# Optimization experiments

Hardware: AMD Instinct MI355X
Metric: run time of the kernel (lower is better)

Reference implementation:

```python
import jax, jax.numpy as jnp
import numpy as np

HEADS = 16
GRID_SIZE = 5      # efficient-KAN default
SPLINE_ORDER = 3   # efficient-KAN default


def _grid(in_features, dtype):
    # grid_range = [-1, 1]
    h = 2.0 / GRID_SIZE
    g = jnp.arange(-SPLINE_ORDER, GRID_SIZE + SPLINE_ORDER + 1, dtype=dtype) * h - 1.0
    return jnp.broadcast_to(g, (in_features, g.shape[0]))  # (in, G)


def _b_splines(x, grid):
    # x: (N, in), grid: (in, G); Cox-de Boor recursion
    xg = x[:, :, None]
    bases = ((xg >= grid[:, :-1]) & (xg < grid[:, 1:])).astype(x.dtype)
    for k in range(1, SPLINE_ORDER + 1):
        bases = ((xg - grid[:, :-(k + 1)]) / (grid[:, k:-1] - grid[:, :-(k + 1)]) * bases[:, :, :-1]
                 + (grid[:, k + 1:] - xg) / (grid[:, k + 1:] - grid[:, 1:-k]) * bases[:, :, 1:])
    return bases  # (N, in, GRID_SIZE + SPLINE_ORDER)


def _kan_linear(x, base_w, spline_w, spline_scaler):
    grid = _grid(x.shape[-1], x.dtype)
    base = jax.nn.silu(x) @ base_w.T                      # (N, out)
    b = _b_splines(x, grid)                               # (N, in, K)
    sw = spline_w * spline_scaler[..., None]              # (out, in, K)
    return base + jnp.einsum('nik,oik->no', b, sw)


def setup_inputs():
    key = jax.random.key(0)
    S, H = 2048, 1024
    hd = H // HEADS
    K = GRID_SIZE + SPLINE_ORDER
    ks = jax.random.split(key, 6)
    x = jax.random.normal(ks[0], (S, H), jnp.float32)
    base_w = jax.random.normal(ks[1], (3 * H, H), jnp.float32) / np.float32(np.sqrt(H))
    spline_w = jax.random.normal(ks[2], (3 * H, H, K), jnp.float32) * 0.1
    spline_scaler = 1.0 + 0.1 * jax.random.normal(ks[3], (3 * H, H), jnp.float32)
    out_w = jax.random.normal(ks[4], (H, H), jnp.float32) / np.float32(np.sqrt(H))
    out_b = jnp.zeros((H,), jnp.float32)
    # RoPE rotation matrix (unit complex), theta = 10000
    t = jnp.arange(S, dtype=jnp.float32)
    freqs = 1.0 / (10000.0 ** (jnp.arange(0, hd, 2, dtype=jnp.float32) / hd))
    ang = jnp.outer(t, freqs)  # (S, hd//2)
    return {"x": x, "base_w": base_w, "spline_w": spline_w,
            "spline_scaler": spline_scaler, "out_w": out_w, "out_b": out_b,
            "rot_cos": jnp.cos(ang), "rot_sin": jnp.sin(ang)}


def reference(x, base_w, spline_w, spline_scaler, out_w, out_b, rot_cos, rot_sin):
    S, H = x.shape
    hd = H // HEADS
    qkv = _kan_linear(x, base_w, spline_w, spline_scaler)          # (S, 3H)
    qkv = qkv.reshape(1, S, HEADS, 3 * hd).transpose(0, 2, 1, 3)   # (1,h,S,3d)
    q, k, v = jnp.split(qkv, 3, axis=-1)                           # each (1,h,S,d)

    def rope(t):
        tp = t.reshape(1, HEADS, S, hd // 2, 2)
        c = rot_cos[None, None]
        s = rot_sin[None, None]
        re = tp[..., 0] * c - tp[..., 1] * s
        im = tp[..., 0] * s + tp[..., 1] * c
        return jnp.stack([re, im], axis=-1).reshape(1, HEADS, S, hd)

    q, k = rope(q), rope(k)
    scores = jnp.einsum('bhqd,bhkd->bhqk', q, k) / np.float32(np.sqrt(hd))
    attn = jax.nn.softmax(scores, axis=-1)
    ctx = jnp.einsum('bhqk,bhkd->bhqd', attn, v)
    ctx = ctx.transpose(0, 2, 1, 3).reshape(1, S, H)
    return ctx @ out_w.T + out_b
```

## Files before the change

kernel.cpp:

```cpp
#include <hip/hip_runtime.h>

typedef unsigned short u16;
typedef __bf16 bf16x8 __attribute__((ext_vector_type(8)));
typedef float f32x4 __attribute__((ext_vector_type(4)));

#define S_LEN 2048
#define NHEADS 16
#define HD 64
#define HDIM 1024
#define QKVN 3072
#define KAUG 9216

__device__ __forceinline__ u16 f2bf(float f) {
  union { float f; unsigned u; } v; v.f = f;
  unsigned r = v.u + 0x7fffu + ((v.u >> 16) & 1u);
  return (u16)(r >> 16);
}

typedef __attribute__((address_space(1))) const unsigned int gas_u32;
typedef __attribute__((address_space(3))) unsigned int las_u32;
__device__ __forceinline__ void gload_lds16(const void* g, void* l) {
  __builtin_amdgcn_global_load_lds((gas_u32*)g, (las_u32*)l, 16, 0, 0);
}

__global__ void prep_a_kernel(const float* __restrict__ x, u16* __restrict__ Aaug) {
  int idx = blockIdx.x * 256 + threadIdx.x;
  int n = idx >> 10, i = idx & 1023;
  float xv = x[idx];
  float sil = xv / (1.0f + __expf(-xv));
  Aaug[(size_t)n * KAUG + i] = f2bf(sil);

  float b[11];
#pragma unroll
  for (int j = 0; j < 11; ++j) {
    float t0 = 0.4f * (float)(j - 3) - 1.0f;
    float t1 = 0.4f * (float)(j - 2) - 1.0f;
    b[j] = (xv >= t0 && xv < t1) ? 1.0f : 0.0f;
  }
#pragma unroll
  for (int k = 1; k <= 3; ++k) {
#pragma unroll
    for (int j = 0; j < 10; ++j) {
      if (j + k < 11) {
        float tj   = 0.4f * (float)(j - 3) - 1.0f;
        float tjk  = tj + 0.4f * (float)k;
        float tj1  = tj + 0.4f;
        float tjk1 = tjk + 0.4f;
        b[j] = (xv - tj) / (tjk - tj) * b[j] + (tjk1 - xv) / (tjk1 - tj1) * b[j + 1];
      }
    }
  }
  u16 t[8];
#pragma unroll
  for (int j = 0; j < 8; ++j) t[j] = f2bf(b[j]);
  uint4 pk;
  pk.x = (unsigned)t[0] | ((unsigned)t[1] << 16);
  pk.y = (unsigned)t[2] | ((unsigned)t[3] << 16);
  pk.z = (unsigned)t[4] | ((unsigned)t[5] << 16);
  pk.w = (unsigned)t[6] | ((unsigned)t[7] << 16);
  *reinterpret_cast<uint4*>(&Aaug[(size_t)n * KAUG + 1024 + i * 8]) = pk;
}

__global__ void prep_w_kernel(const float* __restrict__ bw, const float* __restrict__ sw,
                              const float* __restrict__ sc, u16* __restrict__ Waug) {
  int idx = blockIdx.x * 256 + threadIdx.x;
  int o = idx >> 10, i = idx & 1023;
  Waug[(size_t)o * KAUG + i] = f2bf(bw[idx]);
  float s = sc[idx];
  const float4* sp = reinterpret_cast<const float4*>(sw + (size_t)idx * 8);
  float4 a = sp[0], b = sp[1];
  uint4 pk;
  pk.x = (unsigned)f2bf(a.x * s) | ((unsigned)f2bf(a.y * s) << 16);
  pk.y = (unsigned)f2bf(a.z * s) | ((unsigned)f2bf(a.w * s) << 16);
  pk.z = (unsigned)f2bf(b.x * s) | ((unsigned)f2bf(b.y * s) << 16);
  pk.w = (unsigned)f2bf(b.z * s) | ((unsigned)f2bf(b.w * s) << 16);
  *reinterpret_cast<uint4*>(&Waug[(size_t)o * KAUG + 1024 + i * 8]) = pk;
}

__global__ void prep_ow_kernel(const float* __restrict__ ow, u16* __restrict__ owbf) {
  int idx = blockIdx.x * 256 + threadIdx.x;
  float4 v = reinterpret_cast<const float4*>(ow)[idx];
  uint2 pk;
  pk.x = (unsigned)f2bf(v.x) | ((unsigned)f2bf(v.y) << 16);
  pk.y = (unsigned)f2bf(v.z) | ((unsigned)f2bf(v.w) << 16);
  reinterpret_cast<uint2*>(owbf)[idx] = pk;
}

__global__ __launch_bounds__(256) void gemm_bt(
    const u16* __restrict__ A, const u16* __restrict__ B, float* __restrict__ C,
    int M, int N, int K, int Ksp, const float* __restrict__ bias)
{
  __shared__ u16 As[128 * 32];
  __shared__ u16 Bs[128 * 32];
  const int tid = threadIdx.x;
  const int lane = tid & 63;
  const int w = tid >> 6;
  const int wr = w >> 1, wc = w & 1;
  const int bm = blockIdx.y, bn = blockIdx.x;
  const int row0 = bm * 128, col0 = bn * 128;
  const int lr = lane & 15, lg = lane >> 4;
  const int kbeg = blockIdx.z * Ksp;
  const int kend = kbeg + Ksp;
  float* Cz = C + (size_t)blockIdx.z * M * N;

  f32x4 acc[4][4];
#pragma unroll
  for (int m = 0; m < 4; ++m)
#pragma unroll
    for (int n = 0; n < 4; ++n) acc[m][n] = (f32x4){0.f, 0.f, 0.f, 0.f};

  const int arow = tid >> 2;
  const int kch  = tid & 3;

  for (int k0 = kbeg; k0 < kend; k0 += 32) {
    const u16* ga0 = A + (size_t)(row0 + arow) * K + k0 + kch * 8;
    const u16* ga1 = ga0 + (size_t)64 * K;
    gload_lds16(ga0, &As[tid * 8]);
    gload_lds16(ga1, &As[2048 + tid * 8]);
    const u16* gb0 = B + (size_t)(col0 + arow) * K + k0 + kch * 8;
    const u16* gb1 = gb0 + (size_t)64 * K;
    gload_lds16(gb0, &Bs[tid * 8]);
    gload_lds16(gb1, &Bs[2048 + tid * 8]);
    __syncthreads();

    bf16x8 af[4], bf[4];
#pragma unroll
    for (int m = 0; m < 4; ++m) {
      int r = wr * 64 + m * 16 + lr;
      af[m] = *reinterpret_cast<const bf16x8*>(&As[r * 32 + lg * 8]);
    }
#pragma unroll
    for (int n = 0; n < 4; ++n) {
      int r = wc * 64 + n * 16 + lr;
      bf[n] = *reinterpret_cast<const bf16x8*>(&Bs[r * 32 + lg * 8]);
    }
#pragma unroll
    for (int m = 0; m < 4; ++m)
#pragma unroll
      for (int n = 0; n < 4; ++n)
        acc[m][n] = __builtin_amdgcn_mfma_f32_16x16x32_bf16(af[m], bf[n], acc[m][n], 0, 0, 0);
    __syncthreads();
  }

#pragma unroll
  for (int m = 0; m < 4; ++m) {
    int row = row0 + wr * 64 + m * 16 + lg * 4;
#pragma unroll
    for (int n = 0; n < 4; ++n) {
      int col = col0 + wc * 64 + n * 16 + lr;
      float bv = bias ? bias[col] : 0.f;
#pragma unroll
      for (int j = 0; j < 4; ++j)
        Cz[(size_t)(row + j) * N + col] = acc[m][n][j] + bv;
    }
  }
}

__global__ void rope_kernel(const float* __restrict__ qkv0, const float* __restrict__ qkv1,
                            const float* __restrict__ rc, const float* __restrict__ rs,
                            u16* __restrict__ qro, u16* __restrict__ kro) {
  int idx = blockIdx.x * 256 + threadIdx.x;
  int h = idx >> 16;
  int rem = idx & 65535;
  int s = rem >> 5, i = rem & 31;
  size_t boff = (size_t)s * QKVN + h * 192;
  const float* b0 = qkv0 + boff;
  const float* b1 = qkv1 + boff;
  float q0 = b0[2 * i] + b1[2 * i];
  float q1 = b0[2 * i + 1] + b1[2 * i + 1];
  float k0 = b0[64 + 2 * i] + b1[64 + 2 * i];
  float k1 = b0[64 + 2 * i + 1] + b1[64 + 2 * i + 1];
  float c = rc[s * 32 + i], sn = rs[s * 32 + i];
  size_t ob = ((size_t)(h * S_LEN + s)) * HD + 2 * i;
  qro[ob]     = f2bf((q0 * c - q1 * sn) * 0.125f);
  qro[ob + 1] = f2bf((q0 * sn + q1 * c) * 0.125f);
  kro[ob]     = f2bf(k0 * c - k1 * sn);
  kro[ob + 1] = f2bf(k0 * sn + k1 * c);
}

__global__ void vtrans_kernel(const float* __restrict__ qkv0, const float* __restrict__ qkv1,
                              u16* __restrict__ vT) {
  __shared__ float tile[64][65];
  int h = blockIdx.x >> 5;
  int st = blockIdx.x & 31;
  int s0 = st * 64;
  int t = threadIdx.x;
  int r = t >> 2, c4 = t & 3;
  size_t soff = (size_t)(s0 + r) * QKVN + h * 192 + 128 + c4 * 16;
  const float* src0 = qkv0 + soff;
  const float* src1 = qkv1 + soff;
#pragma unroll
  for (int z = 0; z < 4; ++z) {
    float4 v = *reinterpret_cast<const float4*>(src0 + z * 4);
    float4 u = *reinterpret_cast<const float4*>(src1 + z * 4);
    tile[r][c4 * 16 + z * 4 + 0] = v.x + u.x;
    tile[r][c4 * 16 + z * 4 + 1] = v.y + u.y;
    tile[r][c4 * 16 + z * 4 + 2] = v.z + u.z;
    tile[r][c4 * 16 + z * 4 + 3] = v.w + u.w;
  }
  __syncthreads();
  int d = t >> 2, sc = t & 3;
  u16* dst = vT + ((size_t)(h * 64 + d)) * S_LEN + s0 + sc * 16;
  unsigned wv[8];
#pragma unroll
  for (int z = 0; z < 8; ++z) {
    unsigned lo = f2bf(tile[sc * 16 + 2 * z][d]);
    unsigned hi = f2bf(tile[sc * 16 + 2 * z + 1][d]);
    wv[z] = lo | (hi << 16);
  }
  *reinterpret_cast<uint4*>(dst)     = make_uint4(wv[0], wv[1], wv[2], wv[3]);
  *reinterpret_cast<uint4*>(dst + 8) = make_uint4(wv[4], wv[5], wv[6], wv[7]);
}

__global__ __launch_bounds__(256) void attn_kernel(
    const u16* __restrict__ qro, const u16* __restrict__ kro,
    const u16* __restrict__ vT, u16* __restrict__ ctxb)
{
  __shared__ u16 plds[4][2][16 * 32];
  const int lane = threadIdx.x & 63;
  const int w = threadIdx.x >> 6;
  const int bid = blockIdx.x;
  const int h = bid >> 5;
  const int qt = (bid & 31) * 4 + w;
  const int lr = lane & 15, lg = lane >> 4;

  const u16* qbase = qro + ((size_t)(h * S_LEN + qt * 16 + lr)) * HD + lg * 8;
  bf16x8 qa0 = *reinterpret_cast<const bf16x8*>(qbase);
  bf16x8 qa1 = *reinterpret_cast<const bf16x8*>(qbase + 32);

  float mrow[4], lrow[4];
  f32x4 o[4];
#pragma unroll
  for (int j = 0; j < 4; ++j) { mrow[j] = -3.0e38f; lrow[j] = 0.f; }
#pragma unroll
  for (int n = 0; n < 4; ++n) o[n] = (f32x4){0.f, 0.f, 0.f, 0.f};

  for (int kt = 0; kt < 64; ++kt) {
    const int key0 = kt * 32;
    const u16* kb = kro + ((size_t)(h * S_LEN + key0 + lr)) * HD + lg * 8;
    bf16x8 k00 = *reinterpret_cast<const bf16x8*>(kb);
    bf16x8 k01 = *reinterpret_cast<const bf16x8*>(kb + 32);
    bf16x8 k10 = *reinterpret_cast<const bf16x8*>(kb + (size_t)16 * HD);
    bf16x8 k11 = *reinterpret_cast<const bf16x8*>(kb + (size_t)16 * HD + 32);

    f32x4 s0 = (f32x4){0.f, 0.f, 0.f, 0.f};
    f32x4 s1 = (f32x4){0.f, 0.f, 0.f, 0.f};
    s0 = __builtin_amdgcn_mfma_f32_16x16x32_bf16(qa0, k00, s0, 0, 0, 0);
    s0 = __builtin_amdgcn_mfma_f32_16x16x32_bf16(qa1, k01, s0, 0, 0, 0);
    s1 = __builtin_amdgcn_mfma_f32_16x16x32_bf16(qa0, k10, s1, 0, 0, 0);
    s1 = __builtin_amdgcn_mfma_f32_16x16x32_bf16(qa1, k11, s1, 0, 0, 0);

    float p0[4], p1[4], alpha[4];
#pragma unroll
    for (int j = 0; j < 4; ++j) {
      float v = fmaxf(s0[j], s1[j]);
      v = fmaxf(v, __shfl_xor(v, 1));
      v = fmaxf(v, __shfl_xor(v, 2));
      v = fmaxf(v, __shfl_xor(v, 4));
      v = fmaxf(v, __shfl_xor(v, 8));
      float mn = fmaxf(mrow[j], v);
      float al = __expf(mrow[j] - mn);
      float e0 = __expf(s0[j] - mn);
      float e1 = __expf(s1[j] - mn);
      lrow[j] = lrow[j] * al + e0 + e1;
      mrow[j] = mn;
      alpha[j] = al;
      p0[j] = e0; p1[j] = e1;
    }
#pragma unroll
    for (int n = 0; n < 4; ++n) {
#pragma unroll
      for (int j = 0; j < 4; ++j) o[n][j] *= alpha[j];
    }

    u16* pb = &plds[w][kt & 1][0];
#pragma unroll
    for (int j = 0; j < 4; ++j) {
      pb[(lg * 4 + j) * 32 + lr]      = f2bf(p0[j]);
      pb[(lg * 4 + j) * 32 + 16 + lr] = f2bf(p1[j]);
    }

    bf16x8 pa = *reinterpret_cast<const bf16x8*>(&pb[lr * 32 + lg * 8]);
    const u16* vb = vT + ((size_t)(h * 64 + lr)) * S_LEN + key0 + lg * 8;
#pragma unroll
    for (int n = 0; n < 4; ++n) {
      bf16x8 vf = *reinterpret_cast<const bf16x8*>(vb + (size_t)(n * 16) * S_LEN);
      o[n] = __builtin_amdgcn_mfma_f32_16x16x32_bf16(pa, vf, o[n], 0, 0, 0);
    }
  }

#pragma unroll
  for (int j = 0; j < 4; ++j) {
    float t = lrow[j];
    t += __shfl_xor(t, 1);
    t += __shfl_xor(t, 2);
    t += __shfl_xor(t, 4);
    t += __shfl_xor(t, 8);
    lrow[j] = t;
  }

#pragma unroll
  for (int n = 0; n < 4; ++n) {
    int col = h * 64 + n * 16 + lr;
#pragma unroll
    for (int j = 0; j < 4; ++j) {
      int row = qt * 16 + lg * 4 + j;
      ctxb[(size_t)row * HDIM + col] = f2bf(o[n][j] / lrow[j]);
    }
  }
}

extern "C" void kernel_launch(void* const* d_in, const int* in_sizes, int n_in,
                              void* d_out, int out_size, void* d_ws, size_t ws_size,
                              hipStream_t stream) {
  const float* x   = (const float*)d_in[0];
  const float* bw  = (const float*)d_in[1];
  const float* sw  = (const float*)d_in[2];
  const float* ssc = (const float*)d_in[3];
  const float* ow  = (const float*)d_in[4];
  const float* ob  = (const float*)d_in[5];
  const float* rc  = (const float*)d_in[6];
  const float* rs  = (const float*)d_in[7];
  float* out = (float*)d_out;

  char* ws = (char*)d_ws;
  u16*   Aaug  = (u16*)(ws);
  u16*   Waug  = (u16*)(ws + 37748736);
  float* qkv0  = (float*)(ws + 94371840);
  float* qkv1  = (float*)(ws + 119537664);
  u16*   qro   = (u16*)(ws + 144703488);
  u16*   kro   = (u16*)(ws + 148897792);
  u16*   vT    = (u16*)(ws + 153092096);
  u16*   owbf  = (u16*)(ws + 157286400);
  u16*   ctxb  = (u16*)(ws + 94371840);

  prep_a_kernel<<<8192, 256, 0, stream>>>(x, Aaug);
  prep_w_kernel<<<12288, 256, 0, stream>>>(bw, sw, ssc, Waug);
  prep_ow_kernel<<<1024, 256, 0, stream>>>(ow, owbf);

  gemm_bt<<<dim3(24, 16, 2), 256, 0, stream>>>(Aaug, Waug, qkv0, 2048, 3072, 9216, 4608, nullptr);

  rope_kernel<<<4096, 256, 0, stream>>>(qkv0, qkv1, rc, rs, qro, kro);
  vtrans_kernel<<<512, 256, 0, stream>>>(qkv0, qkv1, vT);

  attn_kernel<<<512, 256, 0, stream>>>(qro, kro, vT, ctxb);

  gemm_bt<<<dim3(8, 16, 1), 256, 0, stream>>>(ctxb, owbf, out, 2048, 1024, 1024, 1024, ob);
}
```

Before: 539.0 us.

## Deepen GEMM K-tile with swizzled LDS, split-K out-proj, and tune attention

The GEMM now stages 64-wide K tiles into LDS with an XOR swizzle, which halves the number of barriers per K and reduces LDS bank conflicts. The output projection becomes split-K over 4 slices, followed by a separate reduce-plus-bias kernel, to raise parallelism on that small GEMM. Several smaller changes come with it: B-spline divisions become multiplies by constants, RoPE uses vectorized loads and stores, attention blocks are remapped across heads with MFMA priority hints, and the softmax normalisation is done with a reciprocal. The split-K path costs an extra partial-buffer round trip through memory and one more kernel launch.

```diff
diff --git a/kernel.cpp b/kernel.cpp
--- a/kernel.cpp
+++ b/kernel.cpp
@@ -39,14 +39,13 @@
   }
 #pragma unroll
   for (int k = 1; k <= 3; ++k) {
+    const float invk = (k == 1) ? 2.5f : (k == 2) ? 1.25f : 0.83333333f;
 #pragma unroll
     for (int j = 0; j < 10; ++j) {
       if (j + k < 11) {
         float tj   = 0.4f * (float)(j - 3) - 1.0f;
-        float tjk  = tj + 0.4f * (float)k;
-        float tj1  = tj + 0.4f;
-        float tjk1 = tjk + 0.4f;
-        b[j] = (xv - tj) / (tjk - tj) * b[j] + (tjk1 - xv) / (tjk1 - tj1) * b[j + 1];
+        float tjk1 = 0.4f * (float)(j + k - 2) - 1.0f;
+        b[j] = ((xv - tj) * b[j] + (tjk1 - xv) * b[j + 1]) * invk;
       }
     }
   }
@@ -88,19 +87,18 @@
 
 __global__ __launch_bounds__(256) void gemm_bt(
     const u16* __restrict__ A, const u16* __restrict__ B, float* __restrict__ C,
-    int M, int N, int K, int Ksp, const float* __restrict__ bias)
+    int M, int N, int K, int Ksp)
 {
-  __shared__ u16 As[128 * 32];
-  __shared__ u16 Bs[128 * 32];
+  __shared__ u16 As[128 * 64];
+  __shared__ u16 Bs[128 * 64];
   const int tid = threadIdx.x;
   const int lane = tid & 63;
   const int w = tid >> 6;
   const int wr = w >> 1, wc = w & 1;
-  const int bm = blockIdx.y, bn = blockIdx.x;
-  const int row0 = bm * 128, col0 = bn * 128;
+  const int row0 = blockIdx.y * 128, col0 = blockIdx.x * 128;
   const int lr = lane & 15, lg = lane >> 4;
   const int kbeg = blockIdx.z * Ksp;
-  const int kend = kbeg + Ksp;
+  const int nsteps = Ksp >> 6;
   float* Cz = C + (size_t)blockIdx.z * M * N;
 
   f32x4 acc[4][4];
@@ -109,36 +107,43 @@
 #pragma unroll
     for (int n = 0; n < 4; ++n) acc[m][n] = (f32x4){0.f, 0.f, 0.f, 0.f};
 
-  const int arow = tid >> 2;
-  const int kch  = tid & 3;
-
-  for (int k0 = kbeg; k0 < kend; k0 += 32) {
-    const u16* ga0 = A + (size_t)(row0 + arow) * K + k0 + kch * 8;
-    const u16* ga1 = ga0 + (size_t)64 * K;
-    gload_lds16(ga0, &As[tid * 8]);
-    gload_lds16(ga1, &As[2048 + tid * 8]);
-    const u16* gb0 = B + (size_t)(col0 + arow) * K + k0 + kch * 8;
-    const u16* gb1 = gb0 + (size_t)64 * K;
-    gload_lds16(gb0, &Bs[tid * 8]);
-    gload_lds16(gb1, &Bs[2048 + tid * 8]);
+  const int srow = tid >> 3;
+  const int c8sw = (tid & 7) ^ (srow & 7);
+  const u16* ga = A + (size_t)(row0 + srow) * K + kbeg + c8sw * 8;
+  const u16* gb = B + (size_t)(col0 + srow) * K + kbeg + c8sw * 8;
+  const size_t rstep = (size_t)32 * K;
+  const int xr = lr & 7;
+
+  for (int ks = 0; ks < nsteps; ++ks) {
+#pragma unroll
+    for (int i = 0; i < 4; ++i) {
+      gload_lds16(ga + i * rstep, &As[i * 2048 + tid * 8]);
+      gload_lds16(gb + i * rstep, &Bs[i * 2048 + tid * 8]);
+    }
+    ga += 64; gb += 64;
     __syncthreads();
 
-    bf16x8 af[4], bf[4];
-#pragma unroll
-    for (int m = 0; m < 4; ++m) {
-      int r = wr * 64 + m * 16 + lr;
-      af[m] = *reinterpret_cast<const bf16x8*>(&As[r * 32 + lg * 8]);
-    }
-#pragma unroll
-    for (int n = 0; n < 4; ++n) {
-      int r = wc * 64 + n * 16 + lr;
-      bf[n] = *reinterpret_cast<const bf16x8*>(&Bs[r * 32 + lg * 8]);
-    }
-#pragma unroll
-    for (int m = 0; m < 4; ++m)
-#pragma unroll
-      for (int n = 0; n < 4; ++n)
-        acc[m][n] = __builtin_amdgcn_mfma_f32_16x16x32_bf16(af[m], bf[n], acc[m][n], 0, 0, 0);
+#pragma unroll
+    for (int kk = 0; kk < 2; ++kk) {
+      bf16x8 af[4], bf[4];
+#pragma unroll
+      for (int m = 0; m < 4; ++m) {
+        int r = wr * 64 + m * 16 + lr;
+        int ch = (kk * 4 + lg) ^ xr;
+        af[m] = *reinterpret_cast<const bf16x8*>(&As[r * 64 + ch * 8]);
+      }
+#pragma unroll
+      for (int n = 0; n < 4; ++n) {
+        int r = wc * 64 + n * 16 + lr;
+        int ch = (kk * 4 + lg) ^ xr;
+        bf[n] = *reinterpret_cast<const bf16x8*>(&Bs[r * 64 + ch * 8]);
+      }
+#pragma unroll
+      for (int m = 0; m < 4; ++m)
+#pragma unroll
+        for (int n = 0; n < 4; ++n)
+          acc[m][n] = __builtin_amdgcn_mfma_f32_16x16x32_bf16(af[m], bf[n], acc[m][n], 0, 0, 0);
+    }
     __syncthreads();
   }
 
@@ -148,12 +153,26 @@
 #pragma unroll
     for (int n = 0; n < 4; ++n) {
       int col = col0 + wc * 64 + n * 16 + lr;
-      float bv = bias ? bias[col] : 0.f;
 #pragma unroll
       for (int j = 0; j < 4; ++j)
-        Cz[(size_t)(row + j) * N + col] = acc[m][n][j] + bv;
-    }
-  }
+        Cz[(size_t)(row + j) * N + col] = acc[m][n][j];
+    }
+  }
+}
+
+__global__ void reduce4_bias_kernel(const float* __restrict__ p, const float* __restrict__ bias,
+                                    float* __restrict__ out) {
+  int idx = blockIdx.x * 256 + threadIdx.x;
+  const float4* p4 = reinterpret_cast<const float4*>(p);
+  const size_t stride4 = (size_t)2048 * 1024 / 4;
+  float4 a = p4[idx], b = p4[idx + stride4], c = p4[idx + 2 * stride4], d = p4[idx + 3 * stride4];
+  float4 bv = reinterpret_cast<const float4*>(bias)[idx & 255];
+  float4 r;
+  r.x = a.x + b.x + c.x + d.x + bv.x;
+  r.y = a.y + b.y + c.y + d.y + bv.y;
+  r.z = a.z + b.z + c.z + d.z + bv.z;
+  r.w = a.w + b.w + c.w + d.w + bv.w;
+  reinterpret_cast<float4*>(out)[idx] = r;
 }
 
 __global__ void rope_kernel(const float* __restrict__ qkv0, const float* __restrict__ qkv1,
@@ -163,19 +182,21 @@
   int h = idx >> 16;
   int rem = idx & 65535;
   int s = rem >> 5, i = rem & 31;
-  size_t boff = (size_t)s * QKVN + h * 192;
-  const float* b0 = qkv0 + boff;
-  const float* b1 = qkv1 + boff;
-  float q0 = b0[2 * i] + b1[2 * i];
-  float q1 = b0[2 * i + 1] + b1[2 * i + 1];
-  float k0 = b0[64 + 2 * i] + b1[64 + 2 * i];
-  float k1 = b0[64 + 2 * i + 1] + b1[64 + 2 * i + 1];
+  size_t boff = (size_t)s * QKVN + h * 192 + 2 * i;
+  float2 q0v = *reinterpret_cast<const float2*>(qkv0 + boff);
+  float2 q1v = *reinterpret_cast<const float2*>(qkv1 + boff);
+  float2 k0v = *reinterpret_cast<const float2*>(qkv0 + boff + 64);
+  float2 k1v = *reinterpret_cast<const float2*>(qkv1 + boff + 64);
+  float q0 = q0v.x + q1v.x, q1 = q0v.y + q1v.y;
+  float k0 = k0v.x + k1v.x, k1 = k0v.y + k1v.y;
   float c = rc[s * 32 + i], sn = rs[s * 32 + i];
   size_t ob = ((size_t)(h * S_LEN + s)) * HD + 2 * i;
-  qro[ob]     = f2bf((q0 * c - q1 * sn) * 0.125f);
-  qro[ob + 1] = f2bf((q0 * sn + q1 * c) * 0.125f);
-  kro[ob]     = f2bf(k0 * c - k1 * sn);
-  kro[ob + 1] = f2bf(k0 * sn + k1 * c);
+  unsigned qpk = (unsigned)f2bf((q0 * c - q1 * sn) * 0.125f) |
+                 ((unsigned)f2bf((q0 * sn + q1 * c) * 0.125f) << 16);
+  unsigned kpk = (unsigned)f2bf(k0 * c - k1 * sn) |
+                 ((unsigned)f2bf(k0 * sn + k1 * c) << 16);
+  *reinterpret_cast<unsigned*>(qro + ob) = qpk;
+  *reinterpret_cast<unsigned*>(kro + ob) = kpk;
 }
 
 __global__ void vtrans_kernel(const float* __restrict__ qkv0, const float* __restrict__ qkv1,
@@ -219,7 +240,7 @@
   __shared__ u16 plds[4][2][16 * 32];
   const int lane = threadIdx.x & 63;
   const int w = threadIdx.x >> 6;
-  const int bid = blockIdx.x;
+  const int bid = (blockIdx.x & 7) * 64 + (blockIdx.x >> 3);
   const int h = bid >> 5;
   const int qt = (bid & 31) * 4 + w;
   const int lr = lane & 15, lg = lane >> 4;
@@ -245,10 +266,12 @@
 
     f32x4 s0 = (f32x4){0.f, 0.f, 0.f, 0.f};
     f32x4 s1 = (f32x4){0.f, 0.f, 0.f, 0.f};
+    __builtin_amdgcn_s_setprio(1);
     s0 = __builtin_amdgcn_mfma_f32_16x16x32_bf16(qa0, k00, s0, 0, 0, 0);
     s0 = __builtin_amdgcn_mfma_f32_16x16x32_bf16(qa1, k01, s0, 0, 0, 0);
     s1 = __builtin_amdgcn_mfma_f32_16x16x32_bf16(qa0, k10, s1, 0, 0, 0);
     s1 = __builtin_amdgcn_mfma_f32_16x16x32_bf16(qa1, k11, s1, 0, 0, 0);
+    __builtin_amdgcn_s_setprio(0);
 
     float p0[4], p1[4], alpha[4];
 #pragma unroll
@@ -282,11 +305,13 @@
 
     bf16x8 pa = *reinterpret_cast<const bf16x8*>(&pb[lr * 32 + lg * 8]);
     const u16* vb = vT + ((size_t)(h * 64 + lr)) * S_LEN + key0 + lg * 8;
+    __builtin_amdgcn_s_setprio(1);
 #pragma unroll
     for (int n = 0; n < 4; ++n) {
       bf16x8 vf = *reinterpret_cast<const bf16x8*>(vb + (size_t)(n * 16) * S_LEN);
       o[n] = __builtin_amdgcn_mfma_f32_16x16x32_bf16(pa, vf, o[n], 0, 0, 0);
     }
+    __builtin_amdgcn_s_setprio(0);
   }
 
 #pragma unroll
@@ -296,7 +321,7 @@
     t += __shfl_xor(t, 2);
     t += __shfl_xor(t, 4);
     t += __shfl_xor(t, 8);
-    lrow[j] = t;
+    lrow[j] = 1.0f / t;
   }
 
 #pragma unroll
@@ -305,7 +330,7 @@
 #pragma unroll
     for (int j = 0; j < 4; ++j) {
       int row = qt * 16 + lg * 4 + j;
-      ctxb[(size_t)row * HDIM + col] = f2bf(o[n][j] / lrow[j]);
+      ctxb[(size_t)row * HDIM + col] = f2bf(o[n][j] * lrow[j]);
     }
   }
 }
@@ -333,17 +358,19 @@
   u16*   vT    = (u16*)(ws + 153092096);
   u16*   owbf  = (u16*)(ws + 157286400);
   u16*   ctxb  = (u16*)(ws + 94371840);
+  float* part  = (float*)(ws + 119537664);
 
   prep_a_kernel<<<8192, 256, 0, stream>>>(x, Aaug);
   prep_w_kernel<<<12288, 256, 0, stream>>>(bw, sw, ssc, Waug);
   prep_ow_kernel<<<1024, 256, 0, stream>>>(ow, owbf);
 
-  gemm_bt<<<dim3(24, 16, 2), 256, 0, stream>>>(Aaug, Waug, qkv0, 2048, 3072, 9216, 4608, nullptr);
+  gemm_bt<<<dim3(24, 16, 2), 256, 0, stream>>>(Aaug, Waug, qkv0, 2048, 3072, 9216, 4608);
 
   rope_kernel<<<4096, 256, 0, stream>>>(qkv0, qkv1, rc, rs, qro, kro);
   vtrans_kernel<<<512, 256, 0, stream>>>(qkv0, qkv1, vT);
 
   attn_kernel<<<512, 256, 0, stream>>>(qro, kro, vT, ctxb);
 
-  gemm_bt<<<dim3(8, 16, 1), 256, 0, stream>>>(ctxb, owbf, out, 2048, 1024, 1024, 1024, ob);
-}
+  gemm_bt<<<dim3(8, 16, 4), 256, 0, stream>>>(ctxb, owbf, part, 2048, 1024, 1024, 256);
+  reduce4_bias_kernel<<<2048, 256, 0, stream>>>(part, ob, out);
+}
```

After: 529.8 us. Within noise of the previous version (-1.7%).
